# Optimization experiments

Hardware: AMD Instinct MI355X
Metric: run time of the kernel (lower is better)

Reference implementation:

```python
import jax, jax.numpy as jnp
import numpy as np

IMG = 640
NUM_CLASSES = 80
B = 8
MAX_BOXES = 32
ALPHA, GAMMA = 0.25, 2.0
EPS = 1e-7


def make_anchors(img_size=IMG):
    strides = [8, 16, 32, 64, 128]
    scales = [2.0 ** 0, 2.0 ** (1.0 / 3.0), 2.0 ** (2.0 / 3.0)]
    ratios = [0.5, 1.0, 2.0]
    out = []
    for s in strides:
        base = 4.0 * s
        fs = img_size // s
        cs = (np.arange(fs) + 0.5) * s
        cy, cx = np.meshgrid(cs, cs, indexing='ij')
        for r in ratios:
            for sc in scales:
                w = base * sc / np.sqrt(r)
                h = base * sc * np.sqrt(r)
                a = np.stack([cx - w / 2, cy - h / 2, cx + w / 2, cy + h / 2], axis=-1).reshape(-1, 4)
                out.append(a)
    return np.concatenate(out, 0).astype(np.float32)  # [76725, 4]


def setup_inputs() -> dict:
    key = jax.random.key(0)
    k1, k2 = jax.random.split(key)
    anchors = jnp.asarray(make_anchors())
    Na = anchors.shape[0]
    cls_pred = jax.random.uniform(k1, (B, NUM_CLASSES, Na), dtype=jnp.float32)
    reg_pred = jax.random.normal(k2, (B, 4, Na), dtype=jnp.float32)
    rng = np.random.RandomState(0)
    x1 = rng.uniform(0, 500, (B, MAX_BOXES)).astype(np.float32)
    y1 = rng.uniform(0, 500, (B, MAX_BOXES)).astype(np.float32)
    w = rng.uniform(10, 140, (B, MAX_BOXES)).astype(np.float32)
    h = rng.uniform(10, 140, (B, MAX_BOXES)).astype(np.float32)
    cls = rng.randint(0, NUM_CLASSES, (B, MAX_BOXES)).astype(np.float32)
    nb = rng.randint(0, MAX_BOXES + 1, (B,))
    pad = np.arange(MAX_BOXES)[None, :] >= nb[:, None]
    cls[pad] = -1.0
    annots = jnp.asarray(np.stack([x1, y1, x1 + w, y1 + h, cls], axis=-1))  # [B,32,5]
    return {"cls_pred": cls_pred, "reg_pred": reg_pred, "annots": annots, "anchors": anchors}


def calc_iou(anchors, boxes):
    # anchors [Na,4], boxes [Nb,4] -> [Na,Nb]
    a_area = ((anchors[:, 2] - anchors[:, 0]) * (anchors[:, 3] - anchors[:, 1]))[:, None]
    b_area = (boxes[:, 2] - boxes[:, 0]) * (boxes[:, 3] - boxes[:, 1])
    iw = jnp.clip(jnp.minimum(anchors[:, 2:3], boxes[:, 2]) - jnp.maximum(anchors[:, 0:1], boxes[:, 0]), 0.0)
    ih = jnp.clip(jnp.minimum(anchors[:, 3:4], boxes[:, 3]) - jnp.maximum(anchors[:, 1:2], boxes[:, 1]), 0.0)
    inter = iw * ih
    union = jnp.clip(a_area + b_area - inter, 1e-7)
    return inter / union


def multibox_loss(cls_pred, reg_pred, annots, anchors):
    aw = anchors[:, 2] - anchors[:, 0]
    ah = anchors[:, 3] - anchors[:, 1]
    acx = anchors[:, 0] + 0.5 * aw
    acy = anchors[:, 1] + 0.5 * ah
    p = jnp.clip(cls_pred, EPS, 1.0 - EPS)
    C = cls_pred.shape[1]

    def per_image(classification, regression, annot):
        valid = annot[:, 4] != -1.0  # [Nb]
        iou = jnp.where(valid[None, :], calc_iou(anchors, annot[:, :4]), -1.0)  # [Na,Nb]
        iou_max = iou.max(axis=1)
        iou_arg = iou.argmax(axis=1)
        positive = iou_max >= 0.5  # [Na]
        num_pos = positive.sum().astype(jnp.float32)
        assigned = annot[iou_arg]  # [Na,5]
        tgt_cls = jnp.where(positive, assigned[:, 4].astype(jnp.int32), -1)
        targets = jax.nn.one_hot(tgt_cls, C, dtype=classification.dtype).T  # [C,Na]
        # focal loss (alpha=0.25, gamma=2) on clamped probabilities
        bce = -(targets * jnp.log(classification) + (1.0 - targets) * jnp.log1p(-classification))
        pt = targets * classification + (1.0 - targets) * (1.0 - classification)
        alpha_t = ALPHA * targets + (1.0 - ALPHA) * (1.0 - targets)
        cls_loss = (alpha_t * (1.0 - pt) ** GAMMA * bce).sum() / jnp.maximum(num_pos, 1.0)
        gw_raw = assigned[:, 2] - assigned[:, 0]
        gh_raw = assigned[:, 3] - assigned[:, 1]
        gcx = assigned[:, 0] + 0.5 * gw_raw
        gcy = assigned[:, 1] + 0.5 * gh_raw
        gw = jnp.clip(gw_raw, 1.0)
        gh = jnp.clip(gh_raw, 1.0)
        dx = (gcx - acx) / aw / 0.1
        dy = (gcy - acy) / ah / 0.1
        dw = jnp.log(gw / aw) / 0.2
        dh = jnp.log(gh / ah) / 0.2
        t = jnp.stack((dx, dy, dw, dh))  # [4,Na]
        diff = jnp.abs(t - regression)
        sl1 = jnp.where(diff <= 1.0 / 9.0, 0.5 * 9.0 * diff * diff, diff - 0.5 / 9.0)
        posf = positive.astype(regression.dtype)[None, :]
        reg_loss = jnp.where(num_pos > 0, (sl1 * posf).sum() / jnp.maximum(4.0 * num_pos, 1.0), 0.0)
        return cls_loss, reg_loss

    cls_l, reg_l = jax.vmap(per_image)(p, reg_pred, annots)
    return cls_l.mean() + reg_l.mean()


def reference(cls_pred, reg_pred, annots, anchors):
    return multibox_loss(cls_pred, reg_pred, annots, anchors)
```

## Files before the change

### kernel.cpp

```cpp
#include <hip/hip_runtime.h>
#include <math.h>


namespace {

constexpr int C  = 80;
constexpr int MB = 32;

__global__ __launch_bounds__(256) void multibox_main(
    const float* __restrict__ cls_pred,
    const float* __restrict__ reg_pred,
    const float* __restrict__ annots,
    const float* __restrict__ anchors,
    double* __restrict__ cls_sum,
    double* __restrict__ reg_sum,
    unsigned int* __restrict__ num_pos,
    int Na)
{
    const int b   = blockIdx.y;
    const int tid = threadIdx.x;
    const int a   = blockIdx.x * 256 + tid;
    const bool inb = (a < Na);

    __shared__ float sann[MB * 5];
    __shared__ float swred[4][3];

    if (tid < MB * 5) sann[tid] = annots[(size_t)b * (MB * 5) + tid];
    __syncthreads();

    float ax1 = 0.f, ay1 = 0.f, ax2 = 0.f, ay2 = 0.f;
    if (inb) {
        const float4 av = *reinterpret_cast<const float4*>(anchors + (size_t)a * 4);
        ax1 = av.x; ay1 = av.y; ax2 = av.z; ay2 = av.w;
    }
    const float a_area = __fmul_rn(__fsub_rn(ax2, ax1), __fsub_rn(ay2, ay1));

    float best = -INFINITY;
    int   bj   = 0;
    for (int j = 0; j < MB; ++j) {
        const float bx1 = sann[j * 5 + 0], by1 = sann[j * 5 + 1];
        const float bx2 = sann[j * 5 + 2], by2 = sann[j * 5 + 3];
        const float bcl = sann[j * 5 + 4];
        float v = -1.0f;
        if (bcl != -1.0f) {
            const float barea = __fmul_rn(__fsub_rn(bx2, bx1), __fsub_rn(by2, by1));
            const float iw = fmaxf(__fsub_rn(fminf(ax2, bx2), fmaxf(ax1, bx1)), 0.0f);
            const float ih = fmaxf(__fsub_rn(fminf(ay2, by2), fmaxf(ay1, by1)), 0.0f);
            const float inter = __fmul_rn(iw, ih);
            const float uni   = fmaxf(__fsub_rn(__fadd_rn(a_area, barea), inter), 1e-7f);
            v = __fdiv_rn(inter, uni);
        }
        if (v > best) { best = v; bj = j; }
    }

    int   tc     = -1;
    float my_reg = 0.0f;
    int   my_pos = 0;
    if (inb && best >= 0.5f) {
        my_pos = 1;
        const float gx1 = sann[bj * 5 + 0], gy1 = sann[bj * 5 + 1];
        const float gx2 = sann[bj * 5 + 2], gy2 = sann[bj * 5 + 3];
        tc = (int)sann[bj * 5 + 4];
        const float aw  = ax2 - ax1,        ah  = ay2 - ay1;
        const float acx = ax1 + 0.5f * aw,  acy = ay1 + 0.5f * ah;
        const float gwr = gx2 - gx1,        ghr = gy2 - gy1;
        const float gcx = gx1 + 0.5f * gwr, gcy = gy1 + 0.5f * ghr;
        const float gw  = fmaxf(gwr, 1.0f), gh  = fmaxf(ghr, 1.0f);
        float t[4];
        t[0] = ((gcx - acx) / aw) / 0.1f;
        t[1] = ((gcy - acy) / ah) / 0.1f;
        t[2] = __logf(gw / aw) / 0.2f;
        t[3] = __logf(gh / ah) / 0.2f;
        const size_t rb = ((size_t)b * 4) * (size_t)Na + (size_t)a;
        #pragma unroll
        for (int k = 0; k < 4; ++k) {
            const float r = reg_pred[rb + (size_t)k * Na];
            const float d = fabsf(t[k] - r);
            my_reg += (d <= (1.0f / 9.0f)) ? 4.5f * d * d : d - (0.5f / 9.0f);
        }
    }

    float csum = 0.0f;
    if (inb) {
        const float* cp = cls_pred + ((size_t)b * C) * (size_t)Na + (size_t)a;
        #pragma unroll 4
        for (int c = 0; c < C; ++c) {
            float p = cp[(size_t)c * Na];
            p = fminf(fmaxf(p, 1e-7f), 1.0f - 1e-7f);
            const float om = 1.0f - p;
            float l;
            if (c == tc) l = 0.25f * om * om * (-__logf(p));
            else         l = 0.75f * p  * p  * (-__logf(om));
            csum += l;
        }
    }

    float rc = csum, rr = my_reg;
    int   rp = my_pos;
    #pragma unroll
    for (int off = 32; off > 0; off >>= 1) {
        rc += __shfl_down(rc, off);
        rr += __shfl_down(rr, off);
        rp += __shfl_down(rp, off);
    }
    const int w = tid >> 6;
    if ((tid & 63) == 0) { swred[w][0] = rc; swred[w][1] = rr; swred[w][2] = (float)rp; }
    __syncthreads();
    if (tid == 0) {
        float tcl = 0.f, trg = 0.f, tps = 0.f;
        #pragma unroll
        for (int i = 0; i < 4; ++i) { tcl += swred[i][0]; trg += swred[i][1]; tps += swred[i][2]; }
        atomicAdd(&cls_sum[b], (double)tcl);
        atomicAdd(&reg_sum[b], (double)trg);
        const unsigned int up = (unsigned int)(tps + 0.5f);
        if (up) atomicAdd(&num_pos[b], up);
    }
}

__global__ void finalize_kernel(const double* __restrict__ cls_sum,
                                const double* __restrict__ reg_sum,
                                const unsigned int* __restrict__ num_pos,
                                float* __restrict__ out, int B)
{
    if (threadIdx.x == 0 && blockIdx.x == 0) {
        double tot = 0.0;
        for (int b = 0; b < B; ++b) {
            const double np = (double)num_pos[b];
            tot += cls_sum[b] / fmax(np, 1.0);
            if (np > 0.0) tot += reg_sum[b] / (4.0 * np);
        }
        out[0] = (float)(tot / (double)B);
    }
}

}

extern "C" void kernel_launch(void* const* d_in, const int* in_sizes, int n_in,
                              void* d_out, int out_size, void* d_ws, size_t ws_size,
                              hipStream_t stream)
{
    const float* cls_pred = (const float*)d_in[0];
    const float* reg_pred = (const float*)d_in[1];
    const float* annots   = (const float*)d_in[2];
    const float* anchors  = (const float*)d_in[3];
    float* out = (float*)d_out;

    const int Na = in_sizes[3] / 4;
    const int B  = in_sizes[2] / (MB * 5);

    double*       cls_sum = (double*)d_ws;
    double*       reg_sum = cls_sum + B;
    unsigned int* num_pos = (unsigned int*)(reg_sum + B);

    hipMemsetAsync(d_ws, 0, (size_t)(2 * B) * sizeof(double) + (size_t)B * sizeof(unsigned int), stream);

    dim3 grid((Na + 255) / 256, B);
    multibox_main<<<grid, 256, 0, stream>>>(cls_pred, reg_pred, annots, anchors,
                                            cls_sum, reg_sum, num_pos, Na);
    finalize_kernel<<<1, 64, 0, stream>>>(cls_sum, reg_sum, num_pos, out, B);
}
```

Measured before the change: 301.8 us.

## Split focal loss into dense negative sum plus sparse positive correction

The per-anchor class loop is replaced by a separate grid-stride kernel that sums the negative-class focal term over all of cls_pred with float4 loads. The assign kernel now computes only a correction (positive minus negative term) for the single target class of each positive anchor. IoU argmax avoids per-box division by cross-multiplying, padded boxes are pre-masked in shared memory, and clamping uses med3. This decouples the streaming load from assignment and improves memory coalescing, at the cost of an extra launch and slightly different float summation order.

```diff
diff --git a/kernel.cpp b/kernel.cpp
--- a/kernel.cpp
+++ b/kernel.cpp
@@ -7,7 +7,11 @@
 constexpr int C  = 80;
 constexpr int MB = 32;
 
-__global__ __launch_bounds__(256) void multibox_main(
+__device__ __forceinline__ float clampp(float p) {
+    return __builtin_amdgcn_fmed3f(p, 1e-7f, (float)(1.0 - 1e-7));
+}
+
+__global__ __launch_bounds__(256) void assign_kernel(
     const float* __restrict__ cls_pred,
     const float* __restrict__ reg_pred,
     const float* __restrict__ annots,
@@ -22,10 +26,20 @@
     const int a   = blockIdx.x * 256 + tid;
     const bool inb = (a < Na);
 
-    __shared__ float sann[MB * 5];
-    __shared__ float swred[4][3];
-
-    if (tid < MB * 5) sann[tid] = annots[(size_t)b * (MB * 5) + tid];
+    __shared__ float4 sbox[MB];
+    __shared__ float2 smeta[MB];
+    __shared__ double swd[4];
+    __shared__ float  swf[4];
+    __shared__ int    swi[4];
+
+    if (tid < MB) {
+        const float* an = annots + ((size_t)b * MB + tid) * 5;
+        float x1 = an[0], y1 = an[1], x2 = an[2], y2 = an[3];
+        const float cl = an[4];
+        if (cl == -1.0f) { x1 = y1 = x2 = y2 = -1e30f; }
+        sbox[tid]  = make_float4(x1, y1, x2, y2);
+        smeta[tid] = make_float2(__fmul_rn(__fsub_rn(x2, x1), __fsub_rn(y2, y1)), cl);
+    }
     __syncthreads();
 
     float ax1 = 0.f, ay1 = 0.f, ax2 = 0.f, ay2 = 0.f;
@@ -35,37 +49,32 @@
     }
     const float a_area = __fmul_rn(__fsub_rn(ax2, ax1), __fsub_rn(ay2, ay1));
 
-    float best = -INFINITY;
-    int   bj   = 0;
+    float ibest = -1.0f, ubest = 1.0f;
+    int   jbest = 0;
+    #pragma unroll
     for (int j = 0; j < MB; ++j) {
-        const float bx1 = sann[j * 5 + 0], by1 = sann[j * 5 + 1];
-        const float bx2 = sann[j * 5 + 2], by2 = sann[j * 5 + 3];
-        const float bcl = sann[j * 5 + 4];
-        float v = -1.0f;
-        if (bcl != -1.0f) {
-            const float barea = __fmul_rn(__fsub_rn(bx2, bx1), __fsub_rn(by2, by1));
-            const float iw = fmaxf(__fsub_rn(fminf(ax2, bx2), fmaxf(ax1, bx1)), 0.0f);
-            const float ih = fmaxf(__fsub_rn(fminf(ay2, by2), fmaxf(ay1, by1)), 0.0f);
-            const float inter = __fmul_rn(iw, ih);
-            const float uni   = fmaxf(__fsub_rn(__fadd_rn(a_area, barea), inter), 1e-7f);
-            v = __fdiv_rn(inter, uni);
-        }
-        if (v > best) { best = v; bj = j; }
-    }
-
-    int   tc     = -1;
-    float my_reg = 0.0f;
-    int   my_pos = 0;
-    if (inb && best >= 0.5f) {
+        const float4 bx = sbox[j];
+        const float2 bm = smeta[j];
+        const float iw    = fmaxf(__fsub_rn(fminf(ax2, bx.z), fmaxf(ax1, bx.x)), 0.0f);
+        const float ih    = fmaxf(__fsub_rn(fminf(ay2, bx.w), fmaxf(ay1, bx.y)), 0.0f);
+        const float inter = __fmul_rn(iw, ih);
+        const float uni   = fmaxf(__fsub_rn(__fadd_rn(a_area, bm.x), inter), 1e-7f);
+        if (inter * ubest > ibest * uni) { ibest = inter; ubest = uni; jbest = j; }
+    }
+
+    double corr   = 0.0;
+    float  my_reg = 0.0f;
+    int    my_pos = 0;
+    if (inb && __fdiv_rn(ibest, ubest) >= 0.5f) {
         my_pos = 1;
-        const float gx1 = sann[bj * 5 + 0], gy1 = sann[bj * 5 + 1];
-        const float gx2 = sann[bj * 5 + 2], gy2 = sann[bj * 5 + 3];
-        tc = (int)sann[bj * 5 + 4];
-        const float aw  = ax2 - ax1,        ah  = ay2 - ay1;
-        const float acx = ax1 + 0.5f * aw,  acy = ay1 + 0.5f * ah;
-        const float gwr = gx2 - gx1,        ghr = gy2 - gy1;
-        const float gcx = gx1 + 0.5f * gwr, gcy = gy1 + 0.5f * ghr;
-        const float gw  = fmaxf(gwr, 1.0f), gh  = fmaxf(ghr, 1.0f);
+        const float4 g  = sbox[jbest];
+        const int    tc = (int)smeta[jbest].y;
+
+        const float aw  = ax2 - ax1,          ah  = ay2 - ay1;
+        const float acx = ax1 + 0.5f * aw,    acy = ay1 + 0.5f * ah;
+        const float gwr = g.z - g.x,          ghr = g.w - g.y;
+        const float gcx = g.x + 0.5f * gwr,   gcy = g.y + 0.5f * ghr;
+        const float gw  = fmaxf(gwr, 1.0f),   gh  = fmaxf(ghr, 1.0f);
         float t[4];
         t[0] = ((gcx - acx) / aw) / 0.1f;
         t[1] = ((gcy - acy) / ah) / 0.1f;
@@ -74,29 +83,23 @@
         const size_t rb = ((size_t)b * 4) * (size_t)Na + (size_t)a;
         #pragma unroll
         for (int k = 0; k < 4; ++k) {
-            const float r = reg_pred[rb + (size_t)k * Na];
-            const float d = fabsf(t[k] - r);
+            const float d = fabsf(t[k] - reg_pred[rb + (size_t)k * Na]);
             my_reg += (d <= (1.0f / 9.0f)) ? 4.5f * d * d : d - (0.5f / 9.0f);
         }
-    }
-
-    float csum = 0.0f;
-    if (inb) {
-        const float* cp = cls_pred + ((size_t)b * C) * (size_t)Na + (size_t)a;
-        #pragma unroll 4
-        for (int c = 0; c < C; ++c) {
-            float p = cp[(size_t)c * Na];
-            p = fminf(fmaxf(p, 1e-7f), 1.0f - 1e-7f);
-            const float om = 1.0f - p;
-            float l;
-            if (c == tc) l = 0.25f * om * om * (-__logf(p));
-            else         l = 0.75f * p  * p  * (-__logf(om));
-            csum += l;
-        }
-    }
-
-    float rc = csum, rr = my_reg;
-    int   rp = my_pos;
+
+        float p = clampp(cls_pred[((size_t)b * C + tc) * (size_t)Na + (size_t)a]);
+        const float om = __fsub_rn(1.0f, p);
+        const float q  = __fsub_rn(1.0f, om);
+        const float Ln = __logf(om);
+        const float Lp = __logf(p);
+        const float neg = -0.75f * __fmul_rn(__fmul_rn(q, q), Ln);
+        const float pos = 0.25f * __fmul_rn(__fmul_rn(om, om), -Lp);
+        corr = (double)pos - (double)neg;
+    }
+
+    double rc = corr;
+    float  rr = my_reg;
+    int    rp = my_pos;
     #pragma unroll
     for (int off = 32; off > 0; off >>= 1) {
         rc += __shfl_down(rc, off);
@@ -104,16 +107,62 @@
         rp += __shfl_down(rp, off);
     }
     const int w = tid >> 6;
-    if ((tid & 63) == 0) { swred[w][0] = rc; swred[w][1] = rr; swred[w][2] = (float)rp; }
+    if ((tid & 63) == 0) { swd[w] = rc; swf[w] = rr; swi[w] = rp; }
     __syncthreads();
     if (tid == 0) {
-        float tcl = 0.f, trg = 0.f, tps = 0.f;
+        double tcorr = 0.0; float treg = 0.f; int tpos = 0;
         #pragma unroll
-        for (int i = 0; i < 4; ++i) { tcl += swred[i][0]; trg += swred[i][1]; tps += swred[i][2]; }
-        atomicAdd(&cls_sum[b], (double)tcl);
-        atomicAdd(&reg_sum[b], (double)trg);
-        const unsigned int up = (unsigned int)(tps + 0.5f);
-        if (up) atomicAdd(&num_pos[b], up);
+        for (int i = 0; i < 4; ++i) { tcorr += swd[i]; treg += swf[i]; tpos += swi[i]; }
+        if (tcorr != 0.0) atomicAdd(&cls_sum[b], tcorr);
+        if (treg  != 0.f) atomicAdd(&reg_sum[b], (double)treg);
+        if (tpos)         atomicAdd(&num_pos[b], (unsigned int)tpos);
+    }
+}
+
+__global__ __launch_bounds__(256) void negsum_kernel(
+    const float* __restrict__ cls_pred,
+    double* __restrict__ cls_sum,
+    int Na)
+{
+    const int b = blockIdx.y;
+    const float4* __restrict__ base =
+        reinterpret_cast<const float4*>(cls_pred + (size_t)b * C * (size_t)Na);
+    const int n4     = (C * Na) >> 2;
+    const int stride = gridDim.x * 256;
+
+    float a0 = 0.f, a1 = 0.f, a2 = 0.f, a3 = 0.f;
+    #pragma unroll 4
+    for (int i = blockIdx.x * 256 + threadIdx.x; i < n4; i += stride) {
+        const float4 v = base[i];
+        {   const float p = clampp(v.x);
+            const float om = __fsub_rn(1.0f, p);
+            const float q  = __fsub_rn(1.0f, om);
+            a0 = fmaf(__fmul_rn(__fmul_rn(q, q), __logf(om)), -0.75f, a0); }
+        {   const float p = clampp(v.y);
+            const float om = __fsub_rn(1.0f, p);
+            const float q  = __fsub_rn(1.0f, om);
+            a1 = fmaf(__fmul_rn(__fmul_rn(q, q), __logf(om)), -0.75f, a1); }
+        {   const float p = clampp(v.z);
+            const float om = __fsub_rn(1.0f, p);
+            const float q  = __fsub_rn(1.0f, om);
+            a2 = fmaf(__fmul_rn(__fmul_rn(q, q), __logf(om)), -0.75f, a2); }
+        {   const float p = clampp(v.w);
+            const float om = __fsub_rn(1.0f, p);
+            const float q  = __fsub_rn(1.0f, om);
+            a3 = fmaf(__fmul_rn(__fmul_rn(q, q), __logf(om)), -0.75f, a3); }
+    }
+    float csum = (a0 + a1) + (a2 + a3);
+
+    #pragma unroll
+    for (int off = 32; off > 0; off >>= 1) csum += __shfl_down(csum, off);
+    __shared__ float sw[4];
+    const int tid = threadIdx.x;
+    const int w = tid >> 6;
+    if ((tid & 63) == 0) sw[w] = csum;
+    __syncthreads();
+    if (tid == 0) {
+        const float tot = (sw[0] + sw[1]) + (sw[2] + sw[3]);
+        atomicAdd(&cls_sum[b], (double)tot);
     }
 }
 
@@ -152,10 +201,16 @@
     double*       reg_sum = cls_sum + B;
     unsigned int* num_pos = (unsigned int*)(reg_sum + B);
 
-    hipMemsetAsync(d_ws, 0, (size_t)(2 * B) * sizeof(double) + (size_t)B * sizeof(unsigned int), stream);
-
-    dim3 grid((Na + 255) / 256, B);
-    multibox_main<<<grid, 256, 0, stream>>>(cls_pred, reg_pred, annots, anchors,
-                                            cls_sum, reg_sum, num_pos, Na);
+    hipMemsetAsync(d_ws, 0,
+                   (size_t)(2 * B) * sizeof(double) + (size_t)B * sizeof(unsigned int),
+                   stream);
+
+    dim3 grid1((Na + 255) / 256, B);
+    assign_kernel<<<grid1, 256, 0, stream>>>(cls_pred, reg_pred, annots, anchors,
+                                             cls_sum, reg_sum, num_pos, Na);
+
+    dim3 grid2(256, B);
+    negsum_kernel<<<grid2, 256, 0, stream>>>(cls_pred, cls_sum, Na);
+
     finalize_kernel<<<1, 64, 0, stream>>>(cls_sum, reg_sum, num_pos, out, B);
 }
```

Result: faster. 294.0 us (-2.6%).
